# Kernel tuning notes

Hardware: AMD Instinct MI355X
Metric: run time of the kernel (lower is better)

Reference implementation:

```python
import jax, jax.numpy as jnp
import numpy as np

EMBED, HID, INSIDE, OUTSIDE, EPS = 128, 64, 4, 8, 1e-5
N_NODES, N_EDGES, BATCH, SEQLEN = 16384, 262144, 64, 21


def _layernorm(x, g, b):
    m = x.mean(-1, keepdims=True)
    v = ((x - m) ** 2).mean(-1, keepdims=True)
    return (x - m) * jax.lax.rsqrt(v + EPS) * g + b


def _lstm_dir(x, Wih, Whh, bih, bhh, reverse):
    # x: [B, L, D] -> h: [B, L, HID]; PyTorch gate order i,f,g,o
    pre = jnp.einsum('bld,gd->blg', x, Wih) + bih + bhh  # [B,L,4H]
    pre = jnp.swapaxes(pre, 0, 1)  # [L,B,4H]
    h0 = jnp.zeros((x.shape[0], HID), x.dtype)

    def step(carry, xt):
        h, c = carry
        gates = xt + h @ Whh.T
        i, f, g, o = jnp.split(gates, 4, axis=-1)
        c = jax.nn.sigmoid(f) * c + jax.nn.sigmoid(i) * jnp.tanh(g)
        h = jax.nn.sigmoid(o) * jnp.tanh(c)
        return (h, c), h

    _, hs = jax.lax.scan(step, (h0, h0), pre, reverse=reverse)
    return jnp.swapaxes(hs, 0, 1)


def setup_inputs():
    key = jax.random.key(0)
    ks = jax.random.split(key, 40)
    f = jnp.float32
    N, E, B, L, D = N_NODES, N_EDGES, BATCH, SEQLEN, EMBED

    def w(k, shape, fan_in):
        return jax.random.normal(k, shape, f) * (1.0 / np.sqrt(fan_in))

    inp = {
        'x': jax.random.normal(ks[0], (N, 2561), f),
        'edge_index': jax.random.randint(ks[1], (2, E), 0, N, jnp.int32),
        'edge_attr': jax.random.normal(ks[2], (E, 3), f),
        # sorted node->graph assignment; every graph id 0..B-1 present
        'batch': ((jnp.arange(N, dtype=jnp.int32) * B) // N).astype(jnp.int32),
        'hotslice': jax.random.normal(ks[3], (B, L, 28), f),
        # randn_like noise tensors from the torch forward, made explicit inputs
        'noise_seqy': jax.random.normal(ks[4], (B, L, D), f),
        'noise_seqz': jax.random.normal(ks[5], (B, L, D), f),
        'noise_sty': jax.random.normal(ks[6], (N, D), f),
        'noise_stz': jax.random.normal(ks[7], (N, D), f),
        # AttnNN params
        'W_esm': w(ks[8], (D, 2560), 2560), 'b_esm': jnp.zeros((D,), f),
        'W_node': w(ks[9], (D, D + 1), D + 1), 'b_node': jnp.zeros((D,), f),
        'W_seq': w(ks[10], (D, 28), 28), 'b_seq': jnp.zeros((D,), f),
        # SeqStructBlock params
        'ln_seq_g': jnp.ones((D,), f), 'ln_seq_b': jnp.zeros((D,), f),
        'ln_st_g': jnp.ones((D,), f), 'ln_st_b': jnp.zeros((D,), f),
        'W_in': w(ks[11], (D, 2 * D + 3), 2 * D + 3), 'b_in': jnp.zeros((D,), f),
        'W_out': w(ks[12], (D, 2 * D + 3), 2 * D + 3), 'b_out': jnp.zeros((D,), f),
        'Wih_f': w(ks[13], (4 * HID, D), HID), 'Whh_f': w(ks[14], (4 * HID, HID), HID),
        'bih_f': jnp.zeros((4 * HID,), f), 'bhh_f': jnp.zeros((4 * HID,), f),
        'Wih_b': w(ks[15], (4 * HID, D), HID), 'Whh_b': w(ks[16], (4 * HID, HID), HID),
        'bih_b': jnp.zeros((4 * HID,), f), 'bhh_b': jnp.zeros((4 * HID,), f),
        # BatchNorm1d (eval mode: running stats)
        'bn_g': jnp.ones((D,), f), 'bn_b': jnp.zeros((D,), f),
        'bn_rm': jnp.zeros((D,), f), 'bn_rv': jnp.ones((D,), f),
    }
    return inp


def reference(x, edge_index, edge_attr, batch, hotslice,
              noise_seqy, noise_seqz, noise_sty, noise_stz,
              W_esm, b_esm, W_node, b_node, W_seq, b_seq,
              ln_seq_g, ln_seq_b, ln_st_g, ln_st_b,
              W_in, b_in, W_out, b_out,
              Wih_f, Whh_f, bih_f, bhh_f, Wih_b, Whh_b, bih_b, bhh_b,
              bn_g, bn_b, bn_rm, bn_rv):
    N = x.shape[0]
    B = hotslice.shape[0]
    src, dst = edge_index[0, 0::2], edge_index[1, 0::2]
    ea_in, ea_out = edge_attr[1::2], edge_attr[0::2]

    def ss(seq, struct):
        # bidirectional LSTM + residual + LayerNorm (dropout = identity, eval)
        hf = _lstm_dir(seq, Wih_f, Whh_f, bih_f, bhh_f, False)
        hb = _lstm_dir(seq, Wih_b, Whh_b, bih_b, bhh_b, True)
        seq = _layernorm(seq + jnp.concatenate([hf, hb], -1), ln_seq_g, ln_seq_b)
        sn = struct
        fs, fd = sn[src], sn[dst]  # [E/2, 128] gathers
        gin = jax.nn.sigmoid(jnp.concatenate([fs, fd, ea_in], -1) @ W_in.T + b_in)
        struct = struct + jax.ops.segment_sum(gin * fd, src, num_segments=N)
        gout = jax.nn.sigmoid(jnp.concatenate([fs, fd, ea_out], -1) @ W_out.T + b_out)
        struct = struct + jax.ops.segment_sum(gout * fs, dst, num_segments=N)
        return seq, _layernorm(struct, ln_st_g, ln_st_b)

    seq0 = hotslice @ W_seq.T + b_seq                       # [B,L,128]
    esm = x[:, 1:] @ W_esm.T + b_esm                        # [N,128]
    struct0 = jnp.concatenate([esm, x[:, :1]], -1) @ W_node.T + b_node  # [N,128]

    def outer(carry):
        sy, sz, ty, tz = carry

        def inner(c, _):
            szc, tzc = c
            return ss(seq0 + sy + szc, struct0 + ty + tzc), None

        (sz, tz), _ = jax.lax.scan(inner, (sz, tz), None, length=INSIDE)
        sy, ty = ss(sy + sz, ty + tz)
        return (sy, sz, ty, tz)

    carry = (noise_seqy, noise_seqz, noise_sty, noise_stz)
    carry, _ = jax.lax.scan(lambda c, _: (outer(c), None), carry, None,
                            length=OUTSIDE - 1)
    sy, sz, ty, tz = outer(carry)

    # middleSelect picks the first node of each consecutive batch run;
    # batch is sorted with every graph id present -> run starts via searchsorted
    starts = jnp.searchsorted(batch, jnp.arange(B, dtype=batch.dtype))
    feat = sy[:, 10, :] + ty[starts]                        # [B,128]
    # BatchNorm1d, eval mode (running stats)
    return (feat - bn_rm) * jax.lax.rsqrt(bn_rv + EPS) * bn_g + bn_b
```

## Files before the change

kernel.cpp:

```cpp
#include <hip/hip_runtime.h>
#include <hip/hip_fp16.h>
#include <math.h>

#define D 128
#define G4 256
#define LSEQ 21
#define EPSF 1e-5f

typedef unsigned short u16;
typedef __attribute__((ext_vector_type(8))) short bf16x8;
typedef __attribute__((ext_vector_type(4))) float f32x4;
typedef __attribute__((ext_vector_type(2))) unsigned u32x2;
typedef __attribute__((ext_vector_type(4))) unsigned u32x4;

#define MFMA16(a,b,c) __builtin_amdgcn_mfma_f32_16x16x32_bf16(a,b,c,0,0,0)

__device__ __forceinline__ float sigf(float x){ return 1.0f/(1.0f+__expf(-x)); }
__device__ __forceinline__ u16 f2bf(float x){
  unsigned u = __float_as_uint(x);
  return (u16)((u + 0x7FFFu + ((u>>16)&1u)) >> 16);
}
__device__ __forceinline__ float bf2f(u16 h){ return __uint_as_float(((unsigned)h)<<16); }
__device__ __forceinline__ unsigned pack_h2(float a, float b){
  __half2 h = __floats2half2_rn(a, b);
  return *(unsigned*)&h;
}
__device__ __forceinline__ float2 unpack_h2(unsigned u){
  __half2 h = *(__half2*)&u;
  return __half22float2(h);
}
__device__ __forceinline__ u16 f2h(float v){ __half h = __float2half(v); return *(u16*)&h; }

__device__ __forceinline__ void edge_acc(u32x4 a, uint2 g, bool valid,
                                         float2 po2, float2 w0, float2 w1, float2 w2,
                                         float& ax, float& ay){
  float e0=__uint_as_float(a.y), e1=__uint_as_float(a.z), e2=__uint_as_float(a.w);
  float2 ps0 = unpack_h2(g.x);
  float2 ps1 = unpack_h2(g.y);
  float gx = po2.x + ps0.x + e0*w0.x + e1*w1.x + e2*w2.x;
  float gy = po2.y + ps1.x + e0*w0.y + e1*w1.y + e2*w2.y;
  float mm = valid ? 1.f : 0.f;
  ax = fmaf(ps0.y*mm, sigf(gx), ax);
  ay = fmaf(ps1.y*mm, sigf(gy), ay);
}

__global__ void k_misc(int* __restrict__ starts, const int* __restrict__ batch, int N, int Bb,
                       float* __restrict__ WEin, float* __restrict__ WEout,
                       const float* __restrict__ W_in, const float* __restrict__ W_out,
                       float* __restrict__ bsum_f, float* __restrict__ bsum_b,
                       const float* __restrict__ bih_f, const float* __restrict__ bhh_f,
                       const float* __restrict__ bih_b, const float* __restrict__ bhh_b){
  int tid = threadIdx.x;
  if (tid < Bb){
    int lo = 0, hi = N;
    while (lo < hi){ int m = (lo+hi)>>1; if (batch[m] < tid) lo = m+1; else hi = m; }
    starts[tid] = lo;
  }
  for (int i = tid; i < 384; i += 256){
    int t = i >> 7, j = i & 127;
    WEin [i] = W_in [(size_t)j*259 + 256 + t];
    WEout[i] = W_out[(size_t)j*259 + 256 + t];
  }
  if (tid < 256){
    bsum_f[tid] = bih_f[tid] + bhh_f[tid];
    bsum_b[tid] = bih_b[tid] + bhh_b[tid];
  }
}

__global__ void k_packB(u16* __restrict__ PB4h, u16* __restrict__ PB4l,
                        u16* __restrict__ PBnh, u16* __restrict__ PBnl,
                        u16* __restrict__ PBEh, u16* __restrict__ PBEl,
                        const float* __restrict__ W_in, const float* __restrict__ W_out,
                        const float* __restrict__ W_node, const float* __restrict__ W_esm){
  int idx = blockIdx.x*256 + threadIdx.x;
  if (idx < 65536){
    int j = idx&7, l=(idx>>3)&63, q=idx>>9;
    int ks = q&3, nt = q>>2;
    int c = nt*16 + (l&15);
    int k = ks*32 + ((l>>4)<<3) + j;
    float v;
    if (c < 128)      v = W_in [(size_t)c*259 + k];
    else if (c < 256) v = W_in [(size_t)(c-128)*259 + 128 + k];
    else if (c < 384) v = W_out[(size_t)(c-256)*259 + k];
    else              v = W_out[(size_t)(c-384)*259 + 128 + k];
    u16 h = f2bf(v);
    PB4h[idx] = h; PB4l[idx] = f2bf(v - bf2f(h));
  } else if (idx < 65536 + 16384){
    int p = idx - 65536;
    int j = p&7, l=(p>>3)&63, q=p>>9;
    int ks = q&3, nt = q>>2;
    int c = nt*16 + (l&15);
    int k = ks*32 + ((l>>4)<<3) + j;
    float v = W_node[(size_t)c*129 + k];
    u16 h = f2bf(v);
    PBnh[p] = h; PBnl[p] = f2bf(v - bf2f(h));
  } else if (idx < 65536 + 16384 + 327680){
    int p = idx - 81920;
    int j = p&7, l=(p>>3)&63, q=p>>9;
    int ks = q%80, nt = q/80;
    int c = nt*16 + (l&15);
    int k = ks*32 + ((l>>4)<<3) + j;
    float v = W_esm[(size_t)c*2560 + k];
    u16 h = f2bf(v);
    PBEh[p] = h; PBEl[p] = f2bf(v - bf2f(h));
  }
}

__global__ void k_seq0(float* __restrict__ seq0, const float* __restrict__ hot,
                       const float* __restrict__ W_seq, const float* __restrict__ b_seq){
  int row = blockIdx.x, j = threadIdx.x;
  const float* h = hot + (size_t)row*28;
  const float* w = W_seq + (size_t)j*28;
  float acc = b_seq[j];
  #pragma unroll
  for (int k = 0; k < 28; k++) acc += h[k]*w[k];
  seq0[(size_t)row*D + j] = acc;
}

__global__ __launch_bounds__(256) void k_esm2(float* __restrict__ struct0, const float* __restrict__ x,
    const u16* __restrict__ PBEh, const u16* __restrict__ PBEl,
    const u16* __restrict__ PBnh, const u16* __restrict__ PBnl,
    const float* __restrict__ b_esm, const float* __restrict__ W_node,
    const float* __restrict__ b_node, int roff){
  __shared__ union {
    struct { u16 xh[32*72], xl[32*72]; } p1;
    struct { u16 Ah[32*136], Al[32*136]; } p2;
  } uu;
  __shared__ float esmF[32*132];
  int tid = threadIdx.x;
  int r0 = (blockIdx.x + roff)*32;
  int w = tid>>6, l = tid&63;
  f32x4 acc[2][2];
  #pragma unroll
  for (int a=0;a<2;a++)
    #pragma unroll
    for (int b=0;b<2;b++) acc[a][b] = (f32x4){0.f,0.f,0.f,0.f};

  float xv[8];
  int rr = tid >> 5, k2i = tid & 31;
  #pragma unroll
  for (int q = 0; q < 4; q++){
    const float* src = x + (size_t)(r0+rr+8*q)*2561 + 1 + k2i*2;
    xv[2*q]   = src[0];
    xv[2*q+1] = src[1];
  }
  for (int kc = 0; kc < 2560; kc += 64){
    __syncthreads();
    unsigned* xh32 = (unsigned*)uu.p1.xh;
    unsigned* xl32 = (unsigned*)uu.p1.xl;
    #pragma unroll
    for (int q = 0; q < 4; q++){
      float v0 = xv[2*q], v1 = xv[2*q+1];
      u16 h0 = f2bf(v0), h1 = f2bf(v1);
      u16 l0 = f2bf(v0 - bf2f(h0)), l1 = f2bf(v1 - bf2f(h1));
      int r = rr + 8*q;
      xh32[r*36 + k2i] = (unsigned)h0 | ((unsigned)h1 << 16);
      xl32[r*36 + k2i] = (unsigned)l0 | ((unsigned)l1 << 16);
    }
    __syncthreads();
    if (kc + 64 < 2560){
      #pragma unroll
      for (int q = 0; q < 4; q++){
        const float* src = x + (size_t)(r0+rr+8*q)*2561 + 1 + kc + 64 + k2i*2;
        xv[2*q]   = src[0];
        xv[2*q+1] = src[1];
      }
    }
    #pragma unroll
    for (int ks = 0; ks < 2; ks++){
      bf16x8 ah[2], al[2];
      #pragma unroll
      for (int rt = 0; rt < 2; rt++){
        int row = rt*16 + (l&15);
        int k = ks*32 + ((l>>4)<<3);
        ah[rt] = *(const bf16x8*)&uu.p1.xh[row*72 + k];
        al[rt] = *(const bf16x8*)&uu.p1.xl[row*72 + k];
      }
      int ksg = (kc>>5) + ks;
      #pragma unroll
      for (int ctl = 0; ctl < 2; ctl++){
        int nt = w*2 + ctl;
        bf16x8 bh = *(const bf16x8*)&PBEh[((size_t)(nt*80 + ksg)*64 + l)*8];
        bf16x8 bl = *(const bf16x8*)&PBEl[((size_t)(nt*80 + ksg)*64 + l)*8];
        #pragma unroll
        for (int rt = 0; rt < 2; rt++){
          acc[rt][ctl] = MFMA16(ah[rt], bh, acc[rt][ctl]);
          acc[rt][ctl] = MFMA16(al[rt], bh, acc[rt][ctl]);
          acc[rt][ctl] = MFMA16(ah[rt], bl, acc[rt][ctl]);
        }
      }
    }
  }
  __syncthreads();
  int cq = l & 15, rqb = (l>>4)*4;
  #pragma unroll
  for (int ctl = 0; ctl < 2; ctl++){
    int coln = (w*2+ctl)*16 + cq;
    float be = b_esm[coln];
    #pragma unroll
    for (int rt = 0; rt < 2; rt++)
      #pragma unroll
      for (int r = 0; r < 4; r++)
        esmF[(rt*16+rqb+r)*132 + coln] = acc[rt][ctl][r] + be;
  }
  __syncthreads();
  {
    unsigned* Ah32 = (unsigned*)uu.p2.Ah;
    unsigned* Al32 = (unsigned*)uu.p2.Al;
    int rr2 = tid >> 6, k2 = tid & 63;
    #pragma unroll
    for (int q = 0; q < 8; q++){
      int r = rr2 + 4*q;
      float v0 = esmF[r*132 + k2*2];
      float v1 = esmF[r*132 + k2*2 + 1];
      u16 h0 = f2bf(v0), h1 = f2bf(v1);
      u16 l0 = f2bf(v0 - bf2f(h0)), l1 = f2bf(v1 - bf2f(h1));
      Ah32[r*68 + k2] = (unsigned)h0 | ((unsigned)h1 << 16);
      Al32[r*68 + k2] = (unsigned)l0 | ((unsigned)l1 << 16);
    }
  }
  __syncthreads();
  f32x4 acc2[2][2];
  #pragma unroll
  for (int a=0;a<2;a++)
    #pragma unroll
    for (int b=0;b<2;b++) acc2[a][b] = (f32x4){0.f,0.f,0.f,0.f};
  #pragma unroll
  for (int ks = 0; ks < 4; ks++){
    bf16x8 ah[2], al[2];
    #pragma unroll
    for (int rt = 0; rt < 2; rt++){
      int row = rt*16 + (l&15);
      int k = ks*32 + ((l>>4)<<3);
      ah[rt] = *(const bf16x8*)&uu.p2.Ah[row*136 + k];
      al[rt] = *(const bf16x8*)&uu.p2.Al[row*136 + k];
    }
    #pragma unroll
    for (int ctl = 0; ctl < 2; ctl++){
      int nt = w*2 + ctl;
      bf16x8 bh = *(const bf16x8*)&PBnh[((size_t)(nt*4 + ks)*64 + l)*8];
      bf16x8 bl = *(const bf16x8*)&PBnl[((size_t)(nt*4 + ks)*64 + l)*8];
      #pragma unroll
      for (int rt = 0; rt < 2; rt++){
        acc2[rt][ctl] = MFMA16(ah[rt], bh, acc2[rt][ctl]);
        acc2[rt][ctl] = MFMA16(al[rt], bh, acc2[rt][ctl]);
        acc2[rt][ctl] = MFMA16(ah[rt], bl, acc2[rt][ctl]);
      }
    }
  }
  #pragma unroll
  for (int ctl = 0; ctl < 2; ctl++){
    int col = (w*2+ctl)*16 + cq;
    float wl = W_node[(size_t)col*129 + 128];
    float bn = b_node[col];
    #pragma unroll
    for (int rt = 0; rt < 2; rt++)
      #pragma unroll
      for (int r = 0; r < 4; r++){
        int row = r0 + rt*16 + rqb + r;
        float x0 = x[(size_t)row*2561];
        struct0[(size_t)row*D + col] = acc2[rt][ctl][r] + x0*wl + bn;
      }
  }
}

__global__ void k_zero2(int* a, int* b, int n){
  int i = blockIdx.x*blockDim.x + threadIdx.x;
  if (i < n){ a[i] = 0; b[i] = 0; }
}
__global__ void k_count(int* cnt_s, int* cnt_d, const int* __restrict__ ei, int E2){
  int e = blockIdx.x*blockDim.x + threadIdx.x;
  if (e < E2){
    atomicAdd(&cnt_s[ei[2*e]], 1);
    atomicAdd(&cnt_d[ei[2*E2 + 2*e]], 1);
  }
}
__global__ __launch_bounds__(1024) void k_scan(const int* __restrict__ cnt, int* __restrict__ offs, int n){
  __shared__ int sh[1024];
  __shared__ int sbase;
  int tid = threadIdx.x;
  if (tid == 0) sbase = 0;
  __syncthreads();
  for (int chunk = 0; chunk < n; chunk += 1024){
    int v = (chunk+tid < n) ? cnt[chunk+tid] : 0;
    sh[tid] = v;
    __syncthreads();
    for (int off = 1; off < 1024; off <<= 1){
      int t = (tid >= off) ? sh[tid-off] : 0;
      __syncthreads();
      sh[tid] += t;
      __syncthreads();
    }
    if (chunk+tid < n) offs[chunk+tid] = sbase + sh[tid] - v;
    __syncthreads();
    if (tid == 0) sbase += sh[1023];
    __syncthreads();
  }
  if (tid == 0) offs[n] = sbase;
}
__global__ void k_copy2(int* cur_s, const int* offs_s, int* cur_d, const int* offs_d, int n){
  int i = blockIdx.x*blockDim.x + threadIdx.x;
  if (i < n){ cur_s[i] = offs_s[i]; cur_d[i] = offs_d[i]; }
}
__global__ void k_fill(const int* __restrict__ ei, const float* __restrict__ eattr, int E2,
                       int* cur_s, int4* __restrict__ adj_s,
                       int* cur_d, int4* __restrict__ adj_d){
  int e = blockIdx.x*blockDim.x + threadIdx.x;
  if (e >= E2) return;
  int s = ei[2*e];
  int d = ei[2*E2 + 2*e];
  const float* ein  = eattr + (size_t)(2*e+1)*3;
  const float* eout = eattr + (size_t)(2*e)*3;
  int ps = atomicAdd(&cur_s[s], 1);
  adj_s[ps] = make_int4(d, __float_as_int(ein[0]),  __float_as_int(ein[1]),  __float_as_int(ein[2]));
  int pd = atomicAdd(&cur_d[d], 1);
  adj_d[pd] = make_int4(s, __float_as_int(eout[0]), __float_as_int(eout[1]), __float_as_int(eout[2]));
}
__global__ void k_pad(int4* __restrict__ adj_s, int4* __restrict__ adj_d, int E2){
  int t = threadIdx.x;
  if (t < 8){
    adj_s[E2+t] = make_int4(0,0,0,0);
    adj_d[E2+t] = make_int4(0,0,0,0);
  }
}

__global__ __launch_bounds__(256) void k_A(
  const float* __restrict__ s0t, const float* __restrict__ ty, const float* __restrict__ tz,
  float* __restrict__ struct_in,
  const u16* __restrict__ PB4h, const u16* __restrict__ PB4l,
  unsigned* __restrict__ G_in, unsigned* __restrict__ G_out,
  unsigned* __restrict__ PownPk,
  const float* __restrict__ b_in, const float* __restrict__ b_out,
  const float* __restrict__ s0s, const float* __restrict__ sy, const float* __restrict__ sz,
  float* __restrict__ seq_in, float* __restrict__ pre_f, float* __restrict__ pre_b,
  const float* __restrict__ Wih_f, const float* __restrict__ Wih_b,
  const float* __restrict__ bsum_f, const float* __restrict__ bsum_b,
  int N, int Bb)
{
  __shared__ union {
    struct { u16 Ah[32*136], Al[32*136]; float Sf[32*132]; } m;
    float sh[LSEQ*128];
  } u;
  int tid = threadIdx.x;
  if ((int)blockIdx.x >= Bb){
    int r0 = (blockIdx.x - Bb)*32;
    const float4* ty4 = (const float4*)(ty + (size_t)r0*D);
    const float4* tz4 = (const float4*)(tz + (size_t)r0*D);
    const float4* s04 = s0t ? (const float4*)(s0t + (size_t)r0*D) : nullptr;
    float4* si4 = (float4*)(struct_in + (size_t)r0*D);
    #pragma unroll
    for (int q = 0; q < 4; q++){
      int i = tid + 256*q;
      int r = i >> 5, k4 = i & 31;
      float4 v = ty4[i];
      float4 z = tz4[i];
      v.x += z.x; v.y += z.y; v.z += z.z; v.w += z.w;
      if (s04){ float4 s = s04[i]; v.x += s.x; v.y += s.y; v.z += s.z; v.w += s.w; }
      si4[i] = v;
      u16 h0 = f2bf(v.x), h1 = f2bf(v.y), h2 = f2bf(v.z), h3 = f2bf(v.w);
      *(ushort4*)&u.m.Ah[r*136 + k4*4] = make_ushort4(h0,h1,h2,h3);
      *(ushort4*)&u.m.Al[r*136 + k4*4] = make_ushort4(
          f2bf(v.x - bf2f(h0)), f2bf(v.y - bf2f(h1)),
          f2bf(v.z - bf2f(h2)), f2bf(v.w - bf2f(h3)));
      *(float4*)&u.m.Sf[r*132 + k4*4] = v;
    }
    __syncthreads();
    int w = tid >> 6, l = tid & 63;
    f32x4 acc[2][8];
    #pragma unroll
    for (int a=0;a<2;a++)
      #pragma unroll
      for (int b=0;b<8;b++) acc[a][b] = (f32x4){0.f,0.f,0.f,0.f};
    #pragma unroll
    for (int ks = 0; ks < 4; ks++){
      bf16x8 ah[2], al[2];
      #pragma unroll
      for (int rt = 0; rt < 2; rt++){
        int row = rt*16 + (l&15);
        int k = ks*32 + ((l>>4)<<3);
        ah[rt] = *(const bf16x8*)&u.m.Ah[row*136 + k];
        al[rt] = *(const bf16x8*)&u.m.Al[row*136 + k];
      }
      #pragma unroll
      for (int ct = 0; ct < 8; ct++){
        int nt = w*8 + ct;
        bf16x8 bh = *(const bf16x8*)&PB4h[((size_t)(nt*4 + ks)*64 + l)*8];
        bf16x8 bl = *(const bf16x8*)&PB4l[((size_t)(nt*4 + ks)*64 + l)*8];
        #pragma unroll
        for (int rt = 0; rt < 2; rt++){
          acc[rt][ct] = MFMA16(ah[rt], bh, acc[rt][ct]);
          acc[rt][ct] = MFMA16(al[rt], bh, acc[rt][ct]);
          acc[rt][ct] = MFMA16(ah[rt], bl, acc[rt][ct]);
        }
      }
    }
    __syncthreads();
    unsigned* stg = (unsigned*)u.m.Ah;
    u16* stg16 = (u16*)u.m.Ah;
    int cq = l & 15, rqb = (l>>4)*4;
    if (w == 1){
      #pragma unroll
      for (int ct = 0; ct < 8; ct++){
        int coln = ct*16 + cq;
        #pragma unroll
        for (int rt = 0; rt < 2; rt++){
          #pragma unroll
          for (int r = 0; r < 4; r++){
            int lr = rt*16 + rqb + r;
            stg[lr*128 + coln] = pack_h2(acc[rt][ct][r], u.m.Sf[lr*132 + coln]);
          }
        }
      }
    }
    __syncthreads();
    {
      uint4* dst = (uint4*)(G_in + (size_t)r0*D);
      const uint4* src = (const uint4*)stg;
      #pragma unroll
      for (int q = 0; q < 4; q++) dst[tid + 256*q] = src[tid + 256*q];
    }
    __syncthreads();
    if (w == 2){
      #pragma unroll
      for (int ct = 0; ct < 8; ct++){
        int coln = ct*16 + cq;
        #pragma unroll
        for (int rt = 0; rt < 2; rt++){
          #pragma unroll
          for (int r = 0; r < 4; r++){
            int lr = rt*16 + rqb + r;
            stg[lr*128 + coln] = pack_h2(acc[rt][ct][r], u.m.Sf[lr*132 + coln]);
          }
        }
      }
    }
    __syncthreads();
    {
      uint4* dst = (uint4*)(G_out + (size_t)r0*D);
      const uint4* src = (const uint4*)stg;
      #pragma unroll
      for (int q = 0; q < 4; q++) dst[tid + 256*q] = src[tid + 256*q];
    }
    __syncthreads();
    if (w == 0 || w == 3){
      const float* bb = (w == 0) ? b_in : b_out;
      int half = (w == 0) ? 0 : 1;
      #pragma unroll
      for (int ct = 0; ct < 8; ct++){
        int coln = ct*16 + cq;
        float bc = bb[coln];
        #pragma unroll
        for (int rt = 0; rt < 2; rt++){
          #pragma unroll
          for (int r = 0; r < 4; r++){
            int lr = rt*16 + rqb + r;
            stg16[(lr*128 + coln)*2 + half] = f2h(acc[rt][ct][r] + bc);
          }
        }
      }
    }
    __syncthreads();
    {
      uint4* dst = (uint4*)(PownPk + (size_t)r0*D);
      const uint4* src = (const uint4*)stg;
      #pragma unroll
      for (int q = 0; q < 4; q++) dst[tid + 256*q] = src[tid + 256*q];
    }
  } else {
    int b = blockIdx.x;
    for (int idx = tid; idx < LSEQ*128; idx += 256){
      size_t off = (size_t)b*LSEQ*128 + idx;
      float v = sy[off] + sz[off];
      if (s0s) v += s0s[off];
      u.sh[idx] = v;
      seq_in[off] = v;
    }
    __syncthreads();
    int g = tid;
    float accf[LSEQ], accb[LSEQ];
    float bf = bsum_f[g], bb = bsum_b[g];
    #pragma unroll
    for (int l = 0; l < LSEQ; l++){ accf[l] = bf; accb[l] = bb; }
    const float* wfp = Wih_f + (size_t)g*128;
    const float* wbp = Wih_b + (size_t)g*128;
    for (int kc = 0; kc < 128; kc += 16){
      float4 wf[4], wb[4];
      #pragma unroll
      for (int q = 0; q < 4; q++){
        wf[q] = *(const float4*)(wfp + kc + 4*q);
        wb[q] = *(const float4*)(wbp + kc + 4*q);
      }
      #pragma unroll
      for (int l = 0; l < LSEQ; l++){
        #pragma unroll
        for (int q = 0; q < 4; q++){
          float4 s4 = *(const float4*)&u.sh[l*128 + kc + 4*q];
          accf[l] += s4.x*wf[q].x + s4.y*wf[q].y + s4.z*wf[q].z + s4.w*wf[q].w;
          accb[l] += s4.x*wb[q].x + s4.y*wb[q].y + s4.z*wb[q].z + s4.w*wb[q].w;
        }
      }
    }
    for (int l = 0; l < LSEQ; l++){
      pre_f[((size_t)b*LSEQ + l)*G4 + g] = accf[l];
      pre_b[((size_t)b*LSEQ + l)*G4 + g] = accb[l];
    }
  }
}

__global__ __launch_bounds__(512) void k_B(
  const unsigned* __restrict__ G_in, const unsigned* __restrict__ G_out,
  const unsigned* __restrict__ PownPk,
  const float* __restrict__ struct_in, float* __restrict__ struct_out,
  const int* __restrict__ offs_s, const int4* __restrict__ adj_s,
  const int* __restrict__ offs_d, const int4* __restrict__ adj_d,
  const float* __restrict__ WEin, const float* __restrict__ WEout,
  const float* __restrict__ ln_st_g, const float* __restrict__ ln_st_b,
  const float* __restrict__ pre_f, const float* __restrict__ pre_b,
  const float* __restrict__ Whh_f, const float* __restrict__ Whh_b,
  const float* __restrict__ seq_in, float* __restrict__ seq_out,
  const float* __restrict__ ln_seq_g, const float* __restrict__ ln_seq_b,
  int N, int Bb)
{
  __shared__ float h_hist[2][LSEQ][64];
  __shared__ float hcur[2][64];
  __shared__ float gsh[2][G4];
  if ((int)blockIdx.x >= Bb){
    int wv = threadIdx.x >> 6, lane = threadIdx.x & 63;
    int n0 = ((blockIdx.x - Bb)*8 + wv)*4;
    const float2* WEi2 = (const float2*)WEin;
    const float2* WEo2 = (const float2*)WEout;
    float2 wi0 = WEi2[lane], wi1 = WEi2[64+lane], wi2 = WEi2[128+lane];
    float2 wo0 = WEo2[lane], wo1 = WEo2[64+lane], wo2 = WEo2[128+lane];
    float2 g2v = ((const float2*)ln_st_g)[lane], be2 = ((const float2*)ln_st_b)[lane];
    const uint2* Gi = (const uint2*)G_in;
    const uint2* Go = (const uint2*)G_out;
    #pragma unroll 1
    for (int n = n0; n < n0+4; ++n){
      u32x2 pw = *((const u32x2*)PownPk + (size_t)n*64 + lane);
      float2 pp0 = unpack_h2(pw.x), pp1 = unpack_h2(pw.y);
      float2 poI = make_float2(pp0.x, pp1.x);
      float2 poO = make_float2(pp0.y, pp1.y);
      float ax = 0.f, ay = 0.f;
      int j0 = __builtin_amdgcn_readfirstlane(offs_s[n]);
      int j1 = __builtin_amdgcn_readfirstlane(offs_s[n+1]);
      for (int jb = j0; jb < j1; jb += 4){
        int rem = j1 - jb;
        const u32x4* ap = (const u32x4*)adj_s + jb;
        u32x4 a0 = ap[0], a1 = ap[1], a2 = ap[2], a3 = ap[3];
        uint2 g0 = Gi[(size_t)a0.x*64 + lane];
        uint2 g1 = Gi[(size_t)a1.x*64 + lane];
        uint2 g2 = Gi[(size_t)a2.x*64 + lane];
        uint2 g3 = Gi[(size_t)a3.x*64 + lane];
        edge_acc(a0, g0, true,  poI, wi0, wi1, wi2, ax, ay);
        edge_acc(a1, g1, rem>1, poI, wi0, wi1, wi2, ax, ay);
        edge_acc(a2, g2, rem>2, poI, wi0, wi1, wi2, ax, ay);
        edge_acc(a3, g3, rem>3, poI, wi0, wi1, wi2, ax, ay);
      }
      j0 = __builtin_amdgcn_readfirstlane(offs_d[n]);
      j1 = __builtin_amdgcn_readfirstlane(offs_d[n+1]);
      for (int jb = j0; jb < j1; jb += 4){
        int rem = j1 - jb;
        const u32x4* ap = (const u32x4*)adj_d + jb;
        u32x4 a0 = ap[0], a1 = ap[1], a2 = ap[2], a3 = ap[3];
        uint2 g0 = Go[(size_t)a0.x*64 + lane];
        uint2 g1 = Go[(size_t)a1.x*64 + lane];
        uint2 g2 = Go[(size_t)a2.x*64 + lane];
        uint2 g3 = Go[(size_t)a3.x*64 + lane];
        edge_acc(a0, g0, true,  poO, wo0, wo1, wo2, ax, ay);
        edge_acc(a1, g1, rem>1, poO, wo0, wo1, wo2, ax, ay);
        edge_acc(a2, g2, rem>2, poO, wo0, wo1, wo2, ax, ay);
        edge_acc(a3, g3, rem>3, poO, wo0, wo1, wo2, ax, ay);
      }
      float2 sn = ((const float2*)struct_in)[(size_t)n*64 + lane];
      float vx = sn.x + ax;
      float vy = sn.y + ay;
      float s = vx+vy, sq = vx*vx + vy*vy;
      #pragma unroll
      for (int o = 32; o; o >>= 1){ s += __shfl_xor(s, o); sq += __shfl_xor(sq, o); }
      float mean = s*(1.f/128.f);
      float inv = rsqrtf(sq*(1.f/128.f) - mean*mean + EPSF);
      float2 o2;
      o2.x = (vx-mean)*inv*g2v.x + be2.x;
      o2.y = (vy-mean)*inv*g2v.y + be2.y;
      ((float2*)struct_out)[(size_t)n*64 + lane] = o2;
    }
  } else {
    int b = blockIdx.x;
    int tid = threadIdx.x;
    int dir = tid >> 8, g = tid & 255;
    const float* Whh = dir ? Whh_b : Whh_f;
    const float* pre = dir ? pre_b : pre_f;
    float w[64];
    #pragma unroll
    for (int q = 0; q < 16; q++){
      float4 t4 = *(const float4*)(Whh + (size_t)g*64 + 4*q);
      w[4*q] = t4.x; w[4*q+1] = t4.y; w[4*q+2] = t4.z; w[4*q+3] = t4.w;
    }
    float c = 0.f;
    for (int t = 0; t < LSEQ; ++t){
      int tt = dir ? (LSEQ-1-t) : t;
      float gate = pre[((size_t)b*LSEQ + tt)*G4 + g];
      if (t > 0){
        #pragma unroll
        for (int q = 0; q < 16; q++){
          float4 h4 = *(const float4*)&hcur[dir][4*q];
          gate += w[4*q]*h4.x + w[4*q+1]*h4.y + w[4*q+2]*h4.z + w[4*q+3]*h4.w;
        }
      }
      gsh[dir][g] = gate;
      __syncthreads();
      if (g < 64){
        float iv = gsh[dir][g], fv = gsh[dir][64+g], gv = gsh[dir][128+g], ov = gsh[dir][192+g];
        c = sigf(fv)*c + sigf(iv)*tanhf(gv);
        float h = sigf(ov)*tanhf(c);
        hcur[dir][g] = h;
        h_hist[dir][tt][g] = h;
      }
      __syncthreads();
    }
    int wv = tid >> 6, lane = tid & 63;
    for (int l = wv; l < LSEQ; l += 8){
      float2 sv = ((const float2*)(seq_in + ((size_t)b*LSEQ + l)*128))[lane];
      float hv0, hv1;
      if (lane < 32){ hv0 = h_hist[0][l][2*lane];    hv1 = h_hist[0][l][2*lane+1]; }
      else          { hv0 = h_hist[1][l][2*lane-64]; hv1 = h_hist[1][l][2*lane-63]; }
      float vx = sv.x + hv0, vy = sv.y + hv1;
      float s = vx+vy, sq = vx*vx + vy*vy;
      #pragma unroll
      for (int o = 32; o; o >>= 1){ s += __shfl_xor(s, o); sq += __shfl_xor(sq, o); }
      float mean = s*(1.f/128.f);
      float inv = rsqrtf(sq*(1.f/128.f) - mean*mean + EPSF);
      float2 g2 = ((const float2*)ln_seq_g)[lane], b2 = ((const float2*)ln_seq_b)[lane];
      float2 o2;
      o2.x = (vx-mean)*inv*g2.x + b2.x;
      o2.y = (vy-mean)*inv*g2.y + b2.y;
      ((float2*)(seq_out + ((size_t)b*LSEQ + l)*128))[lane] = o2;
    }
  }
}

__global__ void k_final(float* __restrict__ out, const float* __restrict__ sy,
                        const float* __restrict__ ty, const int* __restrict__ starts,
                        const float* __restrict__ g, const float* __restrict__ b,
                        const float* __restrict__ rm, const float* __restrict__ rv, int Bb){
  int i = blockIdx.x*blockDim.x + threadIdx.x;
  if (i >= Bb*D) return;
  int bb = i >> 7, d = i & 127;
  float feat = sy[((size_t)bb*LSEQ + 10)*D + d] + ty[(size_t)starts[bb]*D + d];
  out[i] = (feat - rm[d])*rsqrtf(rv[d]+EPSF)*g[d] + b[d];
}

extern "C" void kernel_launch(void* const* d_in, const int* in_sizes, int n_in,
                              void* d_out, int out_size, void* d_ws, size_t ws_size,
                              hipStream_t stream)
{
  const float* x        = (const float*)d_in[0];
  const int*   ei       = (const int*)  d_in[1];
  const float* eattr    = (const float*)d_in[2];
  const int*   batch    = (const int*)  d_in[3];
  const float* hotslice = (const float*)d_in[4];
  const float* nsy      = (const float*)d_in[5];
  const float* nsz      = (const float*)d_in[6];
  const float* nty      = (const float*)d_in[7];
  const float* ntz      = (const float*)d_in[8];
  const float* W_esm    = (const float*)d_in[9];
  const float* b_esm    = (const float*)d_in[10];
  const float* W_node   = (const float*)d_in[11];
  const float* b_node   = (const float*)d_in[12];
  const float* W_seq    = (const float*)d_in[13];
  const float* b_seq    = (const float*)d_in[14];
  const float* ln_seq_g = (const float*)d_in[15];
  const float* ln_seq_b = (const float*)d_in[16];
  const float* ln_st_g  = (const float*)d_in[17];
  const float* ln_st_b  = (const float*)d_in[18];
  const float* W_in     = (const float*)d_in[19];
  const float* b_in     = (const float*)d_in[20];
  const float* W_out    = (const float*)d_in[21];
  const float* b_out    = (const float*)d_in[22];
  const float* Wih_f    = (const float*)d_in[23];
  const float* Whh_f    = (const float*)d_in[24];
  const float* bih_f    = (const float*)d_in[25];
  const float* bhh_f    = (const float*)d_in[26];
  const float* Wih_b    = (const float*)d_in[27];
  const float* Whh_b    = (const float*)d_in[28];
  const float* bih_b    = (const float*)d_in[29];
  const float* bhh_b    = (const float*)d_in[30];
  const float* bn_g     = (const float*)d_in[31];
  const float* bn_b     = (const float*)d_in[32];
  const float* bn_rm    = (const float*)d_in[33];
  const float* bn_rv    = (const float*)d_in[34];

  const int N  = in_sizes[0] / 2561;
  const int E  = in_sizes[1] / 2;
  const int E2 = E / 2;
  const int Bb = in_sizes[4] / (LSEQ*28);
  const int BL = Bb*LSEQ;

  char* p = (char*)d_ws;
  auto alloc = [&](size_t bytes)->void*{
    void* r = (void*)p; p += (bytes + 255) & ~(size_t)255; return r;
  };
  float*    seq0      = (float*)alloc((size_t)BL*D*4);
  float*    sy        = (float*)alloc((size_t)BL*D*4);
  float*    sz        = (float*)alloc((size_t)BL*D*4);
  float*    seq_in    = (float*)alloc((size_t)BL*D*4);
  float*    pre_f     = (float*)alloc((size_t)BL*G4*4);
  float*    pre_b     = (float*)alloc((size_t)BL*G4*4);
  float*    struct0   = (float*)alloc((size_t)N*D*4);
  float*    ty        = (float*)alloc((size_t)N*D*4);
  float*    tz        = (float*)alloc((size_t)N*D*4);
  float*    struct_in = (float*)alloc((size_t)N*D*4);
  unsigned* G_in      = (unsigned*)alloc((size_t)N*D*4);
  unsigned* G_out     = (unsigned*)alloc((size_t)N*D*4);
  unsigned* PownPk    = (unsigned*)alloc((size_t)N*D*4);
  u16*      PB4h      = (u16*)alloc(65536*2);
  u16*      PB4l      = (u16*)alloc(65536*2);
  u16*      PBnh      = (u16*)alloc(16384*2);
  u16*      PBnl      = (u16*)alloc(16384*2);
  u16*      PBEh      = (u16*)alloc(327680*2);
  u16*      PBEl      = (u16*)alloc(327680*2);
  float*    WEin      = (float*)alloc(384*4);
  float*    WEout     = (float*)alloc(384*4);
  float*    bsum_f    = (float*)alloc(256*4);
  float*    bsum_b    = (float*)alloc(256*4);
  int*      starts    = (int*)alloc((size_t)Bb*4);
  int*      cnt_s     = (int*)alloc((size_t)N*4);
  int*      cnt_d     = (int*)alloc((size_t)N*4);
  int*      offs_s    = (int*)alloc((size_t)(N+1)*4);
  int*      offs_d    = (int*)alloc((size_t)(N+1)*4);
  int*      cur_s     = (int*)alloc((size_t)N*4);
  int*      cur_d     = (int*)alloc((size_t)N*4);
  int4*     adj_s     = (int4*)alloc((size_t)(E2+8)*16);
  int4*     adj_d     = (int4*)alloc((size_t)(E2+8)*16);
  (void)ws_size; (void)n_in; (void)out_size;

  hipMemcpyAsync(sy, nsy, (size_t)BL*D*4, hipMemcpyDeviceToDevice, stream);
  hipMemcpyAsync(sz, nsz, (size_t)BL*D*4, hipMemcpyDeviceToDevice, stream);
  hipMemcpyAsync(ty, nty, (size_t)N*D*4, hipMemcpyDeviceToDevice, stream);
  hipMemcpyAsync(tz, ntz, (size_t)N*D*4, hipMemcpyDeviceToDevice, stream);

  k_misc<<<1, 256, 0, stream>>>(starts, batch, N, Bb, WEin, WEout, W_in, W_out,
                                bsum_f, bsum_b, bih_f, bhh_f, bih_b, bhh_b);
  k_packB<<<1600, 256, 0, stream>>>(PB4h, PB4l, PBnh, PBnl, PBEh, PBEl,
                                    W_in, W_out, W_node, W_esm);
  k_seq0<<<BL, 128, 0, stream>>>(seq0, hotslice, W_seq, b_seq);
  k_esm2<<<N/64, 256, 0, stream>>>(struct0, x, PBEh, PBEl, PBnh, PBnl,
                                   b_esm, W_node, b_node, 0);
  k_esm2<<<N/64, 256, 0, stream>>>(struct0, x, PBEh, PBEl, PBnh, PBnl,
                                   b_esm, W_node, b_node, N/64);
  k_zero2<<<(N+255)/256, 256, 0, stream>>>(cnt_s, cnt_d, N);
  k_count<<<(E2+255)/256, 256, 0, stream>>>(cnt_s, cnt_d, ei, E2);
  k_scan<<<1, 1024, 0, stream>>>(cnt_s, offs_s, N);
  k_scan<<<1, 1024, 0, stream>>>(cnt_d, offs_d, N);
  k_copy2<<<(N+255)/256, 256, 0, stream>>>(cur_s, offs_s, cur_d, offs_d, N);
  k_fill<<<(E2+255)/256, 256, 0, stream>>>(ei, eattr, E2, cur_s, adj_s, cur_d, adj_d);
  k_pad<<<1, 64, 0, stream>>>(adj_s, adj_d, E2);

  const int NB_T1 = N/32;
  const int NB_T2 = N/32;

  for (int o = 0; o < 8; ++o){
    for (int it = 0; it < 5; ++it){
      bool inner = (it < 4);
      const float* s0s = inner ? seq0 : nullptr;
      const float* s0t = inner ? struct0 : nullptr;
      float* so = inner ? sz : sy;
      float* to = inner ? tz : ty;
      k_A<<<Bb + NB_T1, 256, 0, stream>>>(s0t, ty, tz, struct_in, PB4h, PB4l,
                                          G_in, G_out, PownPk, b_in, b_out,
                                          s0s, sy, sz, seq_in, pre_f, pre_b,
                                          Wih_f, Wih_b, bsum_f, bsum_b, N, Bb);
      k_B<<<Bb + NB_T2, 512, 0, stream>>>(G_in, G_out, PownPk, struct_in, to,
                                          offs_s, adj_s, offs_d, adj_d,
                                          WEin, WEout, ln_st_g, ln_st_b,
                                          pre_f, pre_b, Whh_f, Whh_b, seq_in, so,
                                          ln_seq_g, ln_seq_b, N, Bb);
    }
  }

  k_final<<<(Bb*D+255)/256, 256, 0, stream>>>((float*)d_out, sy, ty, starts,
                                              bn_g, bn_b, bn_rm, bn_rv, Bb);
}
```

Measured before the change: 4.437 ms.

## Vectorize ESM loads, merge staging barriers, and interleave in/out edge gathers

The ESM projection kernel now loads each row's x slice as two float4 reads per thread instead of scattered float pairs, and runs as a single launch instead of two halves. In k_A, the three output tiles (G_in, G_out, PownPk) are staged in separate shared buffers so all warps write at once and the global stores happen after one barrier, at the cost of extra shared memory that may lower occupancy. In k_B, the source- and destination-edge gather loops are merged into one loop that issues eight gathers per iteration to expose more memory-level parallelism. Exhausted edge lists fall back to the padded entries at index E2.

```diff
diff --git a/kernel.cpp b/kernel.cpp
--- a/kernel.cpp
+++ b/kernel.cpp
@@ -121,14 +121,14 @@
     const u16* __restrict__ PBEh, const u16* __restrict__ PBEl,
     const u16* __restrict__ PBnh, const u16* __restrict__ PBnl,
     const float* __restrict__ b_esm, const float* __restrict__ W_node,
-    const float* __restrict__ b_node, int roff){
+    const float* __restrict__ b_node){
   __shared__ union {
     struct { u16 xh[32*72], xl[32*72]; } p1;
     struct { u16 Ah[32*136], Al[32*136]; } p2;
   } uu;
   __shared__ float esmF[32*132];
   int tid = threadIdx.x;
-  int r0 = (blockIdx.x + roff)*32;
+  int r0 = blockIdx.x*32;
   int w = tid>>6, l = tid&63;
   f32x4 acc[2][2];
   #pragma unroll
@@ -136,35 +136,29 @@
     #pragma unroll
     for (int b=0;b<2;b++) acc[a][b] = (f32x4){0.f,0.f,0.f,0.f};
 
-  float xv[8];
-  int rr = tid >> 5, k2i = tid & 31;
-  #pragma unroll
-  for (int q = 0; q < 4; q++){
-    const float* src = x + (size_t)(r0+rr+8*q)*2561 + 1 + k2i*2;
-    xv[2*q]   = src[0];
-    xv[2*q+1] = src[1];
-  }
+  int rr = tid >> 3, c8 = (tid & 7)*8;
+  const float* xrow = x + (size_t)(r0+rr)*2561 + 1 + c8;
+  float4 xva = *(const float4*)(xrow);
+  float4 xvb = *(const float4*)(xrow + 4);
   for (int kc = 0; kc < 2560; kc += 64){
     __syncthreads();
     unsigned* xh32 = (unsigned*)uu.p1.xh;
     unsigned* xl32 = (unsigned*)uu.p1.xl;
-    #pragma unroll
-    for (int q = 0; q < 4; q++){
-      float v0 = xv[2*q], v1 = xv[2*q+1];
-      u16 h0 = f2bf(v0), h1 = f2bf(v1);
-      u16 l0 = f2bf(v0 - bf2f(h0)), l1 = f2bf(v1 - bf2f(h1));
-      int r = rr + 8*q;
-      xh32[r*36 + k2i] = (unsigned)h0 | ((unsigned)h1 << 16);
-      xl32[r*36 + k2i] = (unsigned)l0 | ((unsigned)l1 << 16);
+    {
+      float vv[8] = {xva.x,xva.y,xva.z,xva.w, xvb.x,xvb.y,xvb.z,xvb.w};
+      #pragma unroll
+      for (int j = 0; j < 4; j++){
+        float v0 = vv[2*j], v1 = vv[2*j+1];
+        u16 h0 = f2bf(v0), h1 = f2bf(v1);
+        u16 l0 = f2bf(v0 - bf2f(h0)), l1 = f2bf(v1 - bf2f(h1));
+        xh32[rr*36 + (c8>>1) + j] = (unsigned)h0 | ((unsigned)h1 << 16);
+        xl32[rr*36 + (c8>>1) + j] = (unsigned)l0 | ((unsigned)l1 << 16);
+      }
     }
     __syncthreads();
     if (kc + 64 < 2560){
-      #pragma unroll
-      for (int q = 0; q < 4; q++){
-        const float* src = x + (size_t)(r0+rr+8*q)*2561 + 1 + kc + 64 + k2i*2;
-        xv[2*q]   = src[0];
-        xv[2*q+1] = src[1];
-      }
+      xva = *(const float4*)(xrow + kc + 64);
+      xvb = *(const float4*)(xrow + kc + 68);
     }
     #pragma unroll
     for (int ks = 0; ks < 2; ks++){
@@ -338,7 +332,8 @@
   int N, int Bb)
 {
   __shared__ union {
-    struct { u16 Ah[32*136], Al[32*136]; float Sf[32*132]; } m;
+    struct { u16 Ah[32*136], Al[32*136]; float Sf[32*132];
+             unsigned stgIn[32*128], stgOut[32*128]; } m;
     float sh[LSEQ*128];
   } u;
   int tid = threadIdx.x;
@@ -395,54 +390,33 @@
       }
     }
     __syncthreads();
-    unsigned* stg = (unsigned*)u.m.Ah;
-    u16* stg16 = (u16*)u.m.Ah;
+    u16* stgPk16 = (u16*)u.m.Ah;
     int cq = l & 15, rqb = (l>>4)*4;
     if (w == 1){
       #pragma unroll
       for (int ct = 0; ct < 8; ct++){
         int coln = ct*16 + cq;
         #pragma unroll
-        for (int rt = 0; rt < 2; rt++){
+        for (int rt = 0; rt < 2; rt++)
           #pragma unroll
           for (int r = 0; r < 4; r++){
             int lr = rt*16 + rqb + r;
-            stg[lr*128 + coln] = pack_h2(acc[rt][ct][r], u.m.Sf[lr*132 + coln]);
+            u.m.stgIn[lr*128 + coln] = pack_h2(acc[rt][ct][r], u.m.Sf[lr*132 + coln]);
           }
-        }
-      }
-    }
-    __syncthreads();
-    {
-      uint4* dst = (uint4*)(G_in + (size_t)r0*D);
-      const uint4* src = (const uint4*)stg;
-      #pragma unroll
-      for (int q = 0; q < 4; q++) dst[tid + 256*q] = src[tid + 256*q];
-    }
-    __syncthreads();
-    if (w == 2){
+      }
+    } else if (w == 2){
       #pragma unroll
       for (int ct = 0; ct < 8; ct++){
         int coln = ct*16 + cq;
         #pragma unroll
-        for (int rt = 0; rt < 2; rt++){
+        for (int rt = 0; rt < 2; rt++)
           #pragma unroll
           for (int r = 0; r < 4; r++){
             int lr = rt*16 + rqb + r;
-            stg[lr*128 + coln] = pack_h2(acc[rt][ct][r], u.m.Sf[lr*132 + coln]);
+            u.m.stgOut[lr*128 + coln] = pack_h2(acc[rt][ct][r], u.m.Sf[lr*132 + coln]);
           }
-        }
-      }
-    }
-    __syncthreads();
-    {
-      uint4* dst = (uint4*)(G_out + (size_t)r0*D);
-      const uint4* src = (const uint4*)stg;
-      #pragma unroll
-      for (int q = 0; q < 4; q++) dst[tid + 256*q] = src[tid + 256*q];
-    }
-    __syncthreads();
-    if (w == 0 || w == 3){
+      }
+    } else {
       const float* bb = (w == 0) ? b_in : b_out;
       int half = (w == 0) ? 0 : 1;
       #pragma unroll
@@ -450,21 +424,29 @@
         int coln = ct*16 + cq;
         float bc = bb[coln];
         #pragma unroll
-        for (int rt = 0; rt < 2; rt++){
+        for (int rt = 0; rt < 2; rt++)
           #pragma unroll
           for (int r = 0; r < 4; r++){
             int lr = rt*16 + rqb + r;
-            stg16[(lr*128 + coln)*2 + half] = f2h(acc[rt][ct][r] + bc);
+            stgPk16[(lr*128 + coln)*2 + half] = f2h(acc[rt][ct][r] + bc);
           }
-        }
       }
     }
     __syncthreads();
     {
-      uint4* dst = (uint4*)(PownPk + (size_t)r0*D);
-      const uint4* src = (const uint4*)stg;
-      #pragma unroll
-      for (int q = 0; q < 4; q++) dst[tid + 256*q] = src[tid + 256*q];
+      uint4* dIn  = (uint4*)(G_in  + (size_t)r0*D);
+      uint4* dOut = (uint4*)(G_out + (size_t)r0*D);
+      uint4* dPk  = (uint4*)(PownPk + (size_t)r0*D);
+      const uint4* sIn  = (const uint4*)u.m.stgIn;
+      const uint4* sOut = (const uint4*)u.m.stgOut;
+      const uint4* sPk  = (const uint4*)stgPk16;
+      #pragma unroll
+      for (int q = 0; q < 4; q++){
+        int i = tid + 256*q;
+        dIn[i]  = sIn[i];
+        dOut[i] = sOut[i];
+        dPk[i]  = sPk[i];
+      }
     }
   } else {
     int b = blockIdx.x;
@@ -519,7 +501,7 @@
   const float* __restrict__ Whh_f, const float* __restrict__ Whh_b,
   const float* __restrict__ seq_in, float* __restrict__ seq_out,
   const float* __restrict__ ln_seq_g, const float* __restrict__ ln_seq_b,
-  int N, int Bb)
+  int N, int Bb, int E2)
 {
   __shared__ float h_hist[2][LSEQ][64];
   __shared__ float hcur[2][64];
@@ -534,6 +516,8 @@
     float2 g2v = ((const float2*)ln_st_g)[lane], be2 = ((const float2*)ln_st_b)[lane];
     const uint2* Gi = (const uint2*)G_in;
     const uint2* Go = (const uint2*)G_out;
+    const u32x4* As = (const u32x4*)adj_s;
+    const u32x4* Ad = (const u32x4*)adj_d;
     #pragma unroll 1
     for (int n = n0; n < n0+4; ++n){
       u32x2 pw = *((const u32x2*)PownPk + (size_t)n*64 + lane);
@@ -541,35 +525,34 @@
       float2 poI = make_float2(pp0.x, pp1.x);
       float2 poO = make_float2(pp0.y, pp1.y);
       float ax = 0.f, ay = 0.f;
-      int j0 = __builtin_amdgcn_readfirstlane(offs_s[n]);
-      int j1 = __builtin_amdgcn_readfirstlane(offs_s[n+1]);
-      for (int jb = j0; jb < j1; jb += 4){
-        int rem = j1 - jb;
-        const u32x4* ap = (const u32x4*)adj_s + jb;
-        u32x4 a0 = ap[0], a1 = ap[1], a2 = ap[2], a3 = ap[3];
-        uint2 g0 = Gi[(size_t)a0.x*64 + lane];
-        uint2 g1 = Gi[(size_t)a1.x*64 + lane];
-        uint2 g2 = Gi[(size_t)a2.x*64 + lane];
-        uint2 g3 = Gi[(size_t)a3.x*64 + lane];
-        edge_acc(a0, g0, true,  poI, wi0, wi1, wi2, ax, ay);
-        edge_acc(a1, g1, rem>1, poI, wi0, wi1, wi2, ax, ay);
-        edge_acc(a2, g2, rem>2, poI, wi0, wi1, wi2, ax, ay);
-        edge_acc(a3, g3, rem>3, poI, wi0, wi1, wi2, ax, ay);
-      }
-      j0 = __builtin_amdgcn_readfirstlane(offs_d[n]);
-      j1 = __builtin_amdgcn_readfirstlane(offs_d[n+1]);
-      for (int jb = j0; jb < j1; jb += 4){
-        int rem = j1 - jb;
-        const u32x4* ap = (const u32x4*)adj_d + jb;
-        u32x4 a0 = ap[0], a1 = ap[1], a2 = ap[2], a3 = ap[3];
-        uint2 g0 = Go[(size_t)a0.x*64 + lane];
-        uint2 g1 = Go[(size_t)a1.x*64 + lane];
-        uint2 g2 = Go[(size_t)a2.x*64 + lane];
-        uint2 g3 = Go[(size_t)a3.x*64 + lane];
-        edge_acc(a0, g0, true,  poO, wo0, wo1, wo2, ax, ay);
-        edge_acc(a1, g1, rem>1, poO, wo0, wo1, wo2, ax, ay);
-        edge_acc(a2, g2, rem>2, poO, wo0, wo1, wo2, ax, ay);
-        edge_acc(a3, g3, rem>3, poO, wo0, wo1, wo2, ax, ay);
+      int js0 = __builtin_amdgcn_readfirstlane(offs_s[n]);
+      int js1 = __builtin_amdgcn_readfirstlane(offs_s[n+1]);
+      int jd0 = __builtin_amdgcn_readfirstlane(offs_d[n]);
+      int jd1 = __builtin_amdgcn_readfirstlane(offs_d[n+1]);
+      int jbs = js0, jbd = jd0;
+      while (jbs < js1 || jbd < jd1){
+        int bs = (jbs < js1) ? jbs : E2;
+        int bd = (jbd < jd1) ? jbd : E2;
+        u32x4 as0 = As[bs], as1 = As[bs+1], as2 = As[bs+2], as3 = As[bs+3];
+        u32x4 ad0 = Ad[bd], ad1 = Ad[bd+1], ad2 = Ad[bd+2], ad3 = Ad[bd+3];
+        uint2 gs0 = Gi[(size_t)as0.x*64 + lane];
+        uint2 gs1 = Gi[(size_t)as1.x*64 + lane];
+        uint2 gs2 = Gi[(size_t)as2.x*64 + lane];
+        uint2 gs3 = Gi[(size_t)as3.x*64 + lane];
+        uint2 gd0 = Go[(size_t)ad0.x*64 + lane];
+        uint2 gd1 = Go[(size_t)ad1.x*64 + lane];
+        uint2 gd2 = Go[(size_t)ad2.x*64 + lane];
+        uint2 gd3 = Go[(size_t)ad3.x*64 + lane];
+        int rs = js1 - jbs, rd = jd1 - jbd;
+        edge_acc(as0, gs0, rs>0, poI, wi0, wi1, wi2, ax, ay);
+        edge_acc(as1, gs1, rs>1, poI, wi0, wi1, wi2, ax, ay);
+        edge_acc(as2, gs2, rs>2, poI, wi0, wi1, wi2, ax, ay);
+        edge_acc(as3, gs3, rs>3, poI, wi0, wi1, wi2, ax, ay);
+        edge_acc(ad0, gd0, rd>0, poO, wo0, wo1, wo2, ax, ay);
+        edge_acc(ad1, gd1, rd>1, poO, wo0, wo1, wo2, ax, ay);
+        edge_acc(ad2, gd2, rd>2, poO, wo0, wo1, wo2, ax, ay);
+        edge_acc(ad3, gd3, rd>3, poO, wo0, wo1, wo2, ax, ay);
+        jbs += 4; jbd += 4;
       }
       float2 sn = ((const float2*)struct_in)[(size_t)n*64 + lane];
       float vx = sn.x + ax;
@@ -744,10 +727,8 @@
   k_packB<<<1600, 256, 0, stream>>>(PB4h, PB4l, PBnh, PBnl, PBEh, PBEl,
                                     W_in, W_out, W_node, W_esm);
   k_seq0<<<BL, 128, 0, stream>>>(seq0, hotslice, W_seq, b_seq);
-  k_esm2<<<N/64, 256, 0, stream>>>(struct0, x, PBEh, PBEl, PBnh, PBnl,
-                                   b_esm, W_node, b_node, 0);
-  k_esm2<<<N/64, 256, 0, stream>>>(struct0, x, PBEh, PBEl, PBnh, PBnl,
-                                   b_esm, W_node, b_node, N/64);
+  k_esm2<<<N/32, 256, 0, stream>>>(struct0, x, PBEh, PBEl, PBnh, PBnl,
+                                   b_esm, W_node, b_node);
   k_zero2<<<(N+255)/256, 256, 0, stream>>>(cnt_s, cnt_d, N);
   k_count<<<(E2+255)/256, 256, 0, stream>>>(cnt_s, cnt_d, ei, E2);
   k_scan<<<1, 1024, 0, stream>>>(cnt_s, offs_s, N);
@@ -774,7 +755,7 @@
                                           offs_s, adj_s, offs_d, adj_d,
                                           WEin, WEout, ln_st_g, ln_st_b,
                                           pre_f, pre_b, Whh_f, Whh_b, seq_in, so,
-                                          ln_seq_g, ln_seq_b, N, Bb);
+                                          ln_seq_g, ln_seq_b, N, Bb, E2);
     }
   }
 
```

After: 4.501 ms. Within noise of the previous version (+1.4%).
